# Kernel optimization log

Measured on AMD Instinct MI355X. Metric: run time of the kernel, lower is better.

Reference implementation:

```python
import jax, jax.numpy as jnp
import numpy as np

V, D, Q = 50000, 300, 200  # vocab, word_embedding_dim, query_vector_dim
ALPHA = 0.2  # LeakyReLU negative slope


def _gat(h, W, a):
    # h: [N, D]; full adjacency of ones -> mask is a no-op, softmax over all pairs
    d = a.shape[0] // 2
    Wh = h @ W                                        # [N, D]
    e = jax.nn.leaky_relu(Wh @ a[:d] + (Wh @ a[d:]).T, ALPHA)  # [N, N]
    att = jax.nn.softmax(e, axis=1)                   # [N, N]
    return jax.nn.elu(att @ Wh)                       # [N, D]


def _additive_attention(x, lin_w, lin_b, query):
    # x: [B, S, D] -> [B, D]
    temp = jnp.tanh(x @ lin_w.T + lin_b)              # [B, S, Q]
    w = jax.nn.softmax(temp @ query, axis=1)          # [B, S, 1]
    return jnp.sum(x * w, axis=1)


def _news_encode(titles, emb, W, a, lin_w, lin_b, query):
    # titles: [B, L] int; dropout p=0 (eval)
    v = emb[titles]                                   # [B, L, D]
    b, l, d = v.shape
    g = _gat(v.reshape(b * l, d), W, a).reshape(b, l, d)
    return _additive_attention(g, lin_w, lin_b, query)  # [B, D]


def setup_inputs() -> dict:
    key = jax.random.key(0)
    ks = jax.random.split(key, 13)
    B, C, H, L = 64, 5, 50, 32
    f = jnp.float32
    return {
        "candidate_titles": jax.random.randint(ks[0], (B, C, L), 0, V, dtype=jnp.int32),
        "clicked_titles": jax.random.randint(ks[1], (B, H, L), 0, V, dtype=jnp.int32),
        "emb": jax.random.normal(ks[2], (V, D), f) * 0.1,
        "news_W": jax.random.normal(ks[3], (D, D), f) * (1.0 / np.sqrt(D)),
        "news_a": jax.random.normal(ks[4], (2 * D, 1), f) * (1.0 / np.sqrt(2 * D)),
        "news_lin_w": jax.random.normal(ks[5], (Q, D), f) * (1.0 / np.sqrt(D)),
        "news_lin_b": jnp.zeros((Q,), f),
        "news_query": jax.random.normal(ks[6], (Q, 1), f) * (1.0 / np.sqrt(Q)),
        "user_W": jax.random.normal(ks[7], (D, D), f) * (1.0 / np.sqrt(D)),
        "user_a": jax.random.normal(ks[8], (2 * D, 1), f) * (1.0 / np.sqrt(2 * D)),
        "user_lin_w": jax.random.normal(ks[9], (Q, D), f) * (1.0 / np.sqrt(D)),
        "user_lin_b": jnp.zeros((Q,), f),
        "user_query": jax.random.normal(ks[10], (Q, 1), f) * (1.0 / np.sqrt(Q)),
    }


def reference(candidate_titles, clicked_titles, emb, news_W, news_a,
              news_lin_w, news_lin_b, news_query, user_W, user_a,
              user_lin_w, user_lin_b, user_query):
    enc = lambda t: _news_encode(t, emb, news_W, news_a, news_lin_w, news_lin_b, news_query)
    # per-news-item encoding (each item gets its own full-batch GAT)
    cand = jax.vmap(enc)(candidate_titles.transpose(1, 0, 2)).transpose(1, 0, 2)   # [B, C, D]
    clicked = jax.vmap(enc)(clicked_titles.transpose(1, 0, 2)).transpose(1, 0, 2)  # [B, H, D]
    # user encoder: GAT over flattened [B*H, D] with full adjacency
    b, h, d = clicked.shape
    g = _gat(clicked.reshape(b * h, d), user_W, user_a).reshape(b, h, d)
    user = _additive_attention(g, user_lin_w, user_lin_b, user_query)              # [B, D]
    # dot-product click predictor
    return jnp.einsum('bcd,bd->bc', cand, user)                                    # [B, C]
```

## Files before the change

kernel.cpp:

```cpp
#include <hip/hip_runtime.h>
#include <hip/hip_bf16.h>

#define BN_B 64
#define NC 5
#define NH 50
#define NL 32
#define DD 300
#define QQ 200
#define NVOC 50000
#define NGAT 55
#define NROW 2048
#define NUSR 3200
#define NUSR_PAD 3328
#define CW 304
#define NT_NEWS 128
#define NT_USER 208
#define NB_NEWS 128
#define NB_USER 200
#define GSTR 320
#define NTILES_N 13
#define KTILES 10
#define BPELT (NTILES_N * KTILES * 64)
#define WNT 19
#define WKT 10
#define WPELT (WNT * WKT * 64)
#define KTBYTES (NTILES_N * 64 * 16)
#define KTCHUNK (KTBYTES / 16)

typedef short bf16x8 __attribute__((ext_vector_type(8)));
typedef short bf16x4 __attribute__((ext_vector_type(4)));
typedef float f32x4 __attribute__((ext_vector_type(4)));

static __device__ __forceinline__ float bf2f(short s) {
  return __uint_as_float(((unsigned)(unsigned short)s) << 16);
}

__global__ __launch_bounds__(256) void k_packW(const float* __restrict__ W0,
                                               const float* __restrict__ W1,
                                               __hip_bfloat16* __restrict__ h0,
                                               __hip_bfloat16* __restrict__ l0,
                                               __hip_bfloat16* __restrict__ h1,
                                               __hip_bfloat16* __restrict__ l1) {
  const float* Wm = blockIdx.y ? W1 : W0;
  __hip_bfloat16* Bhi = blockIdx.y ? h1 : h0;
  __hip_bfloat16* Blo = blockIdx.y ? l1 : l0;
  int e = blockIdx.x * 256 + threadIdx.x;
  if (e >= WPELT) return;
  int lane = e & 63, nt = (e >> 6) % WNT, kt = (e >> 6) / WNT;
  int n = nt * 16 + (lane & 15);
  int k0 = kt * 32 + (lane >> 4) * 8;
  __hip_bfloat16 hv[8], lv[8];
#pragma unroll
  for (int j = 0; j < 8; ++j) {
    int k = k0 + j;
    float v = (k < DD && n < DD) ? Wm[(size_t)k * DD + n] : 0.f;
    __hip_bfloat16 h = __float2bfloat16(v);
    hv[j] = h;
    lv[j] = __float2bfloat16(v - __bfloat162float(h));
  }
  *(bf16x8*)(Bhi + (size_t)e * 8) = *(const bf16x8*)hv;
  *(bf16x8*)(Blo + (size_t)e * 8) = *(const bf16x8*)lv;
}

__global__ __launch_bounds__(256) void k_packB(const float* __restrict__ lw0,
                                               const float* __restrict__ lw1,
                                               __hip_bfloat16* __restrict__ B0,
                                               __hip_bfloat16* __restrict__ B1) {
  const float* lw = blockIdx.y ? lw1 : lw0;
  __hip_bfloat16* Bp = blockIdx.y ? B1 : B0;
  int e = blockIdx.x * 256 + threadIdx.x;
  if (e >= BPELT) return;
  int lane = e & 63, nt = (e >> 6) % NTILES_N, kt = (e >> 6) / NTILES_N;
  int n = nt * 16 + (lane & 15);
  int k0 = kt * 32 + (lane >> 4) * 8;
  __hip_bfloat16 vals[8];
#pragma unroll
  for (int j = 0; j < 8; ++j) {
    int k = k0 + j;
    float v = (n < QQ && k < DD) ? lw[(size_t)n * DD + k] : 0.f;
    vals[j] = __float2bfloat16(v);
  }
  *(bf16x8*)(Bp + (size_t)e * 8) = *(const bf16x8*)vals;
}

__global__ __launch_bounds__(256) void k_gemm_mfma(const float* __restrict__ A,
                                                   const __hip_bfloat16* __restrict__ Bhi,
                                                   const __hip_bfloat16* __restrict__ Blo,
                                                   const float* __restrict__ avec,
                                                   float* __restrict__ C,
                                                   float* __restrict__ s1o,
                                                   float* __restrict__ s2o, int M) {
  const int tid = threadIdx.x;
  const int wave = tid >> 6, lane = tid & 63;
  const int quad = lane >> 4, l16 = lane & 15;
  const int rowA = blockIdx.x * 64 + wave * 16 + l16;
  const float* ar = A + (size_t)rowA * DD;
  f32x4 acc[WNT];
#pragma unroll
  for (int nt = 0; nt < WNT; ++nt) acc[nt] = (f32x4){0.f, 0.f, 0.f, 0.f};

  for (int kt = 0; kt < WKT; ++kt) {
    const int k0 = kt * 32 + quad * 8;
    float av[8];
    if (rowA < M && k0 + 8 <= DD) {
      float4 v0 = *(const float4*)(ar + k0);
      float4 v1 = *(const float4*)(ar + k0 + 4);
      av[0] = v0.x; av[1] = v0.y; av[2] = v0.z; av[3] = v0.w;
      av[4] = v1.x; av[5] = v1.y; av[6] = v1.z; av[7] = v1.w;
    } else {
#pragma unroll
      for (int j = 0; j < 8; ++j) {
        int k = k0 + j;
        av[j] = (rowA < M && k < DD) ? ar[k] : 0.f;
      }
    }
    __hip_bfloat16 hv[8], lv[8];
#pragma unroll
    for (int j = 0; j < 8; ++j) {
      __hip_bfloat16 h = __float2bfloat16(av[j]);
      hv[j] = h;
      lv[j] = __float2bfloat16(av[j] - __bfloat162float(h));
    }
    const bf16x8 ah = *(const bf16x8*)hv;
    const bf16x8 al = *(const bf16x8*)lv;
    const bf16x8* bh = (const bf16x8*)Bhi + (size_t)(kt * WNT) * 64 + lane;
    const bf16x8* bl = (const bf16x8*)Blo + (size_t)(kt * WNT) * 64 + lane;
#pragma unroll
    for (int nt = 0; nt < WNT; ++nt) {
      bf16x8 bhf = bh[nt * 64], blf = bl[nt * 64];
      acc[nt] = __builtin_amdgcn_mfma_f32_16x16x32_bf16(ah, bhf, acc[nt], 0, 0, 0);
      acc[nt] = __builtin_amdgcn_mfma_f32_16x16x32_bf16(al, bhf, acc[nt], 0, 0, 0);
      acc[nt] = __builtin_amdgcn_mfma_f32_16x16x32_bf16(ah, blf, acc[nt], 0, 0, 0);
    }
  }
  const int mbase = blockIdx.x * 64 + wave * 16 + quad * 4;
#pragma unroll
  for (int nt = 0; nt < WNT; ++nt) {
    int n = nt * 16 + l16;
    if (n < DD) {
#pragma unroll
      for (int r = 0; r < 4; ++r) {
        int mr = mbase + r;
        if (mr < M) C[(size_t)mr * DD + n] = acc[nt][r];
      }
    }
  }
  float a1v[WNT], a2v[WNT];
#pragma unroll
  for (int nt = 0; nt < WNT; ++nt) {
    int n = nt * 16 + l16;
    a1v[nt] = (n < DD) ? avec[n] : 0.f;
    a2v[nt] = (n < DD) ? avec[DD + n] : 0.f;
  }
#pragma unroll
  for (int r = 0; r < 4; ++r) {
    float p1 = 0.f, p2 = 0.f;
#pragma unroll
    for (int nt = 0; nt < WNT; ++nt) {
      p1 = fmaf(acc[nt][r], a1v[nt], p1);
      p2 = fmaf(acc[nt][r], a2v[nt], p2);
    }
    p1 += __shfl_xor(p1, 1, 64); p1 += __shfl_xor(p1, 2, 64);
    p1 += __shfl_xor(p1, 4, 64); p1 += __shfl_xor(p1, 8, 64);
    p2 += __shfl_xor(p2, 1, 64); p2 += __shfl_xor(p2, 2, 64);
    p2 += __shfl_xor(p2, 4, 64); p2 += __shfl_xor(p2, 8, 64);
    int mr = mbase + r;
    if (l16 == 0 && mr < M) { s1o[mr] = p1; s2o[mr] = p2; }
  }
}

__global__ __launch_bounds__(1024) void k_sort2(const int* __restrict__ cand,
                                                const int* __restrict__ clicked,
                                                const float* __restrict__ s2src,
                                                const float* __restrict__ s1src,
                                                int* __restrict__ perm,
                                                float* __restrict__ E1, float* __restrict__ E02,
                                                int* __restrict__ rlist, float* __restrict__ rs1,
                                                int* __restrict__ boff,
                                                int mode, int N, int SZ, int Epad, int NB) {
  __shared__ float sval[4096];
  __shared__ int spay[4096];
  __shared__ int cnt[224];
  __shared__ int ofs[224];
  const int m = blockIdx.x;
  const int tid = threadIdx.x;
  int* perm_g = perm + (size_t)m * Epad;
  float* E1_g = E1 + (size_t)m * Epad;
  float* E02_g = E02 + (size_t)m * Epad;

  for (int i = tid; i < SZ; i += 1024) {
    float v; int p;
    if (mode == 0) {
      int b = i >> 5, l = i & 31;
      int tok = (m < NC) ? cand[b * (NC * NL) + m * NL + l]
                         : clicked[b * (NH * NL) + (m - NC) * NL + l];
      v = s2src[tok]; p = tok;
    } else {
      if (i < N) { v = s2src[i]; p = i; } else { v = __builtin_inff(); p = 0; }
    }
    sval[i] = v; spay[i] = p;
  }
  __syncthreads();
  for (int k = 2; k <= SZ; k <<= 1) {
    for (int j = k >> 1; j > 0; j >>= 1) {
      for (int i = tid; i < SZ; i += 1024) {
        int ixj = i ^ j;
        if (ixj > i) {
          bool asc = ((i & k) == 0);
          float a = sval[i], bb = sval[ixj];
          bool sw = asc ? (a > bb) : (a < bb);
          if (sw) {
            sval[i] = bb; sval[ixj] = a;
            int t = spay[i]; spay[i] = spay[ixj]; spay[ixj] = t;
          }
        }
      }
      __syncthreads();
    }
  }
  for (int i = tid; i < Epad; i += 1024) {
    E1_g[i] = (i < N) ? expf(sval[i]) : 0.f;
    E02_g[i] = (i < N) ? expf(0.2f * sval[i]) : 0.f;
    perm_g[i] = spay[i];
  }
  __syncthreads();
  for (int t = tid; t <= NB; t += 1024) cnt[t] = 0;
  __syncthreads();
  int* kil = spay;
  for (int r = tid; r < N; r += 1024) {
    int tok;
    if (mode == 0) {
      int b = r >> 5, l = r & 31;
      tok = (m < NC) ? cand[b * (NC * NL) + m * NL + l]
                     : clicked[b * (NH * NL) + (m - NC) * NL + l];
    } else tok = r;
    float tau = -s1src[tok];
    int lo = 0, hi = N;
    while (lo < hi) { int mid = (lo + hi) >> 1; if (sval[mid] <= tau) lo = mid + 1; else hi = mid; }
    kil[r] = lo;
    atomicAdd(&cnt[lo >> 4], 1);
  }
  __syncthreads();
  if (tid == 0) {
    int run = 0;
    for (int t = 0; t <= NB; ++t) { ofs[t] = run; run += cnt[t]; cnt[t] = ofs[t]; }
  }
  __syncthreads();
  int* rlist_g = rlist + (size_t)m * N;
  float* rs1_g = rs1 + (size_t)m * N;
  for (int r = tid; r < N; r += 1024) {
    int ki = kil[r];
    int pos = atomicAdd(&cnt[ki >> 4], 1);
    rlist_g[pos] = (ki << 16) | r;
    int tok;
    if (mode == 0) {
      int b = r >> 5, l = r & 31;
      tok = (m < NC) ? cand[b * (NC * NL) + m * NL + l]
                     : clicked[b * (NH * NL) + (m - NC) * NL + l];
    } else tok = r;
    rs1_g[pos] = s1src[tok];
  }
  int* boff_g = boff + (size_t)m * (NB + 2);
  for (int t = tid; t <= NB; t += 1024) boff_g[t] = ofs[t];
  if (tid == 0) boff_g[NB + 1] = N;
}

__global__ __launch_bounds__(320) void k_scan(const float* __restrict__ base,
                                              const int* __restrict__ perm,
                                              const float* __restrict__ E1,
                                              const float* __restrict__ E02,
                                              float* __restrict__ C1, float* __restrict__ C02,
                                              float* __restrict__ T1, float* __restrict__ T02,
                                              int Epad, int cstride, int nkc) {
  const int g = blockIdx.y, kc = blockIdx.x;
  const int col = threadIdx.x;
  const int* perm_g = perm + (size_t)g * Epad;
  const float* E1_g = E1 + (size_t)g * Epad;
  const float* E02_g = E02 + (size_t)g * Epad;
  float* C1_g = C1 + (size_t)g * cstride * CW;
  float* C02_g = C02 + (size_t)g * cstride * CW;
  const bool datacol = (col < DD);
  const float wden = (col == DD) ? 1.f : 0.f;
  float acc1 = 0.f, acc2 = 0.f;
  const int k0 = kc * 256;
#pragma unroll 8
  for (int kk = 0; kk < 256; ++kk) {
    int k = k0 + kk;
    int tok = perm_g[k];
    float e1 = E1_g[k], e02 = E02_g[k];
    float w = datacol ? base[(size_t)tok * DD + col] : wden;
    acc1 = fmaf(e1, w, acc1);
    acc2 = fmaf(e02, w, acc2);
    if ((kk & 15) == 15) {
      int t = (k + 1) >> 4;
      if (col < CW) { C1_g[(size_t)t * CW + col] = acc1; C02_g[(size_t)t * CW + col] = acc2; }
    }
  }
  if (col < CW) {
    T1[((size_t)g * nkc + kc) * CW + col] = acc1;
    T02[((size_t)g * nkc + kc) * CW + col] = acc2;
  }
}

__global__ __launch_bounds__(320) void k_rows2(
    const float* __restrict__ base,
    const int* __restrict__ perm, const float* __restrict__ E1, const float* __restrict__ E02,
    const float* __restrict__ C1, const float* __restrict__ C02,
    const float* __restrict__ T1, const float* __restrict__ T02,
    const int* __restrict__ rlist, const float* __restrict__ rs1,
    const int* __restrict__ boff,
    __hip_bfloat16* __restrict__ gout,
    int N, int NT, int Epad, int NB, int nkc) {
  __shared__ float U1[16][CW];
  __shared__ float U02[16][CW];
  __shared__ int tokL[16];
  __shared__ float e1L[16], e02L[16];
  const int t = blockIdx.x, g = blockIdx.y;
  const int col = threadIdx.x;
  const int* boff_g = boff + (size_t)g * (NB + 2);
  const int i0 = boff_g[t], i1 = boff_g[t + 1];
  if (i0 >= i1) return;
  const int* perm_g = perm + (size_t)g * Epad;
  const float* E1_g = E1 + (size_t)g * Epad;
  const float* E02_g = E02 + (size_t)g * Epad;
  if (col < 16) {
    int idx = t * 16 + col;
    bool v = idx < N;
    tokL[col] = v ? perm_g[idx] : 0;
    e1L[col] = v ? E1_g[idx] : 0.f;
    e02L[col] = v ? E02_g[idx] : 0.f;
  }
  __syncthreads();
  if (col < CW) {
    const int kc = (t == 0) ? 0 : ((t - 1) >> 4);
    float tot1 = 0.f, pre1 = 0.f, pre02 = 0.f;
#pragma unroll
    for (int c = 0; c < 13; ++c) {
      if (c < nkc) {
        float tv = T1[((size_t)g * nkc + c) * CW + col];
        tot1 += tv;
        if (c < kc) {
          pre1 += tv;
          pre02 += T02[((size_t)g * nkc + c) * CW + col];
        }
      }
    }
    if (t > 0) {
      pre1 += C1[((size_t)g * (NT + 1) + t) * CW + col];
      pre02 += C02[((size_t)g * (NT + 1) + t) * CW + col];
    }
    float u1 = tot1 - pre1;
    float u02 = pre02;
    float wv[16];
#pragma unroll
    for (int j = 0; j < 16; ++j) {
      if (col < DD) wv[j] = ((t * 16 + j) < N) ? base[(size_t)tokL[j] * DD + col] : 0.f;
      else wv[j] = (col == DD) ? 1.f : 0.f;
    }
#pragma unroll
    for (int j = 0; j < 16; ++j) {
      U1[j][col] = u1; U02[j][col] = u02;
      u1 = fmaf(-e1L[j], wv[j], u1);
      u02 = fmaf(e02L[j], wv[j], u02);
    }
  }
  __syncthreads();
  const int wave = col >> 6, lane = col & 63;
  const int* rlist_g = rlist + (size_t)g * N;
  const float* rs1_g = rs1 + (size_t)g * N;
  for (int i = i0 + wave; i < i1; i += 5) {
    int e = rlist_g[i];
    int r = e & 0xffff, nr = (e >> 16) & 15;
    float s1 = rs1_g[i];
    float es1 = expf(s1), es02 = expf(0.2f * s1);
    float den = es1 * U1[nr][DD] + es02 * U02[nr][DD];
    float rden = 1.f / den;
    __hip_bfloat16* gr = gout + ((size_t)g * N + r) * GSTR;
#pragma unroll
    for (int cc = 0; cc < 2; ++cc) {
      int ch = lane + 64 * cc;
      if (ch < 80) {
        short ov[4];
        if (ch < 75) {
          const int c0 = ch * 4;
          float4 u1v = *(const float4*)&U1[nr][c0];
          float4 u2v = *(const float4*)&U02[nr][c0];
          float n0 = fmaf(es1, u1v.x, es02 * u2v.x) * rden;
          float n1 = fmaf(es1, u1v.y, es02 * u2v.y) * rden;
          float n2 = fmaf(es1, u1v.z, es02 * u2v.z) * rden;
          float n3 = fmaf(es1, u1v.w, es02 * u2v.w) * rden;
          float g0 = (n0 > 0.f) ? n0 : expm1f(n0);
          float g1 = (n1 > 0.f) ? n1 : expm1f(n1);
          float g2 = (n2 > 0.f) ? n2 : expm1f(n2);
          float g3 = (n3 > 0.f) ? n3 : expm1f(n3);
          __hip_bfloat16 h0 = __float2bfloat16(g0), h1 = __float2bfloat16(g1);
          __hip_bfloat16 h2 = __float2bfloat16(g2), h3 = __float2bfloat16(g3);
          ov[0] = *(short*)&h0; ov[1] = *(short*)&h1;
          ov[2] = *(short*)&h2; ov[3] = *(short*)&h3;
        } else {
          ov[0] = ov[1] = ov[2] = ov[3] = 0;
        }
        *(bf16x4*)(gr + ch * 4) = *(bf16x4*)ov;
      }
    }
  }
}

__global__ __launch_bounds__(512) void k_logits_attn(
    const __hip_bfloat16* __restrict__ g, const __hip_bfloat16* __restrict__ Bp,
    const float* __restrict__ lin_b, const float* __restrict__ query,
    float* __restrict__ cand_enc, float* __restrict__ clicked_enc) {
  __shared__ __align__(16) short Bs[2][NTILES_N * 512];
  __shared__ float lg[128];
  __shared__ float wgt[128];
  __shared__ float accw[8][GSTR];
  const int tid = threadIdx.x;
  const int wave = tid >> 6, lane = tid & 63;
  const int quad = lane >> 4, l16 = lane & 15;
  const int m = blockIdx.x >> 4;
  const int rbase = (blockIdx.x & 15) * 128;
  const __hip_bfloat16* grow =
      g + ((size_t)m * NROW + rbase + wave * 16 + l16) * GSTR + quad * 8;
  bf16x8 afr[KTILES];
#pragma unroll
  for (int kt = 0; kt < KTILES; ++kt) afr[kt] = *(const bf16x8*)(grow + kt * 32);

  const float4* bsrc = (const float4*)Bp;
  float4* bdst0 = (float4*)&Bs[0][0];
  float4* bdst1 = (float4*)&Bs[1][0];
  float4 st0, st1;
  {
    st0 = bsrc[tid];
    if (tid < KTCHUNK - 512) st1 = bsrc[512 + tid];
    bdst0[tid] = st0;
    if (tid < KTCHUNK - 512) bdst0[512 + tid] = st1;
    st0 = bsrc[KTCHUNK + tid];
    if (tid < KTCHUNK - 512) st1 = bsrc[KTCHUNK + 512 + tid];
  }
  __syncthreads();
  f32x4 acc[NTILES_N];
#pragma unroll
  for (int nt = 0; nt < NTILES_N; ++nt) acc[nt] = (f32x4){0.f, 0.f, 0.f, 0.f};
  int c = 0;
  for (int kt = 0; kt < KTILES; ++kt) {
    const bf16x8* bp = (const bf16x8*)&Bs[c][0] + lane;
#pragma unroll
    for (int nt = 0; nt < NTILES_N; ++nt)
      acc[nt] = __builtin_amdgcn_mfma_f32_16x16x32_bf16(afr[kt], bp[nt * 64], acc[nt], 0, 0, 0);
    if (kt < KTILES - 1) {
      __syncthreads();
      float4* bd = c ? bdst0 : bdst1;
      bd[tid] = st0;
      if (tid < KTCHUNK - 512) bd[512 + tid] = st1;
      if (kt < KTILES - 2) {
        st0 = bsrc[(size_t)(kt + 2) * KTCHUNK + tid];
        if (tid < KTCHUNK - 512) st1 = bsrc[(size_t)(kt + 2) * KTCHUNK + 512 + tid];
      }
      __syncthreads();
      c ^= 1;
    }
  }
  float part[4] = {0.f, 0.f, 0.f, 0.f};
#pragma unroll
  for (int nt = 0; nt < NTILES_N; ++nt) {
    const int n = nt * 16 + l16;
    const float qv = (n < QQ) ? query[n] : 0.f;
    const float bv = (n < QQ) ? lin_b[n] : 0.f;
#pragma unroll
    for (int r = 0; r < 4; ++r)
      part[r] = fmaf(tanhf(acc[nt][r] + bv), qv, part[r]);
  }
#pragma unroll
  for (int r = 0; r < 4; ++r) {
    float p = part[r];
    p += __shfl_xor(p, 1, 64); p += __shfl_xor(p, 2, 64);
    p += __shfl_xor(p, 4, 64); p += __shfl_xor(p, 8, 64);
    if (l16 == 0) lg[wave * 16 + quad * 4 + r] = p;
  }
  __syncthreads();
  if (tid < 128) {
    float v = lg[tid];
    float mx = v;
    mx = fmaxf(mx, __shfl_xor(mx, 1, 64)); mx = fmaxf(mx, __shfl_xor(mx, 2, 64));
    mx = fmaxf(mx, __shfl_xor(mx, 4, 64)); mx = fmaxf(mx, __shfl_xor(mx, 8, 64));
    mx = fmaxf(mx, __shfl_xor(mx, 16, 64));
    float e = expf(v - mx), sm = e;
    sm += __shfl_xor(sm, 1, 64); sm += __shfl_xor(sm, 2, 64);
    sm += __shfl_xor(sm, 4, 64); sm += __shfl_xor(sm, 8, 64);
    sm += __shfl_xor(sm, 16, 64);
    wgt[tid] = e / sm;
  }
  __syncthreads();
  const float w = wgt[wave * 16 + l16];
#pragma unroll
  for (int kt = 0; kt < KTILES; ++kt) {
#pragma unroll
    for (int j = 0; j < 8; ++j) {
      float v = bf2f(afr[kt][j]) * w;
      v += __shfl_xor(v, 1, 64); v += __shfl_xor(v, 2, 64);
      v += __shfl_xor(v, 4, 64); v += __shfl_xor(v, 8, 64);
      if (l16 == 0) accw[wave][kt * 32 + quad * 8 + j] = v;
    }
  }
  __syncthreads();
  const int b0 = rbase >> 5;
  for (int idx = tid; idx < 4 * DD; idx += 512) {
    int j = idx / DD, cc = idx % DD;
    float* op = (m < NC) ? (cand_enc + ((size_t)(b0 + j) * NC + m) * DD)
                         : (clicked_enc + ((size_t)(b0 + j) * NH + (m - NC)) * DD);
    op[cc] = accw[2 * j][cc] + accw[2 * j + 1][cc];
  }
}

__global__ __launch_bounds__(256) void k_user_attn(
    const __hip_bfloat16* __restrict__ g, const __hip_bfloat16* __restrict__ Bp,
    const float* __restrict__ lin_b, const float* __restrict__ query,
    const float* __restrict__ cand_enc, float* __restrict__ out) {
  __shared__ float lg[64];
  __shared__ float wgt[64];
  __shared__ float accw[4][GSTR];
  __shared__ float uenc[CW];
  __shared__ float wred[4];
  const int b = blockIdx.x, tid = threadIdx.x;
  const int wave = tid >> 6, lane = tid & 63;
  const int quad = lane >> 4, l16 = lane & 15;
  const int rl = wave * 16 + l16;
  const int rclamp = (rl < NH) ? rl : 0;
  const __hip_bfloat16* grow = g + ((size_t)b * NH + rclamp) * GSTR + quad * 8;
  bf16x8 afr[KTILES];
#pragma unroll
  for (int kt = 0; kt < KTILES; ++kt) afr[kt] = *(const bf16x8*)(grow + kt * 32);
  f32x4 acc[NTILES_N];
#pragma unroll
  for (int nt = 0; nt < NTILES_N; ++nt) acc[nt] = (f32x4){0.f, 0.f, 0.f, 0.f};
  for (int kt = 0; kt < KTILES; ++kt) {
    const bf16x8* bp = (const bf16x8*)Bp + (size_t)kt * NTILES_N * 64 + lane;
#pragma unroll
    for (int nt = 0; nt < NTILES_N; ++nt)
      acc[nt] = __builtin_amdgcn_mfma_f32_16x16x32_bf16(afr[kt], bp[nt * 64], acc[nt], 0, 0, 0);
  }
  float part[4] = {0.f, 0.f, 0.f, 0.f};
#pragma unroll
  for (int nt = 0; nt < NTILES_N; ++nt) {
    const int n = nt * 16 + l16;
    const float qv = (n < QQ) ? query[n] : 0.f;
    const float bv = (n < QQ) ? lin_b[n] : 0.f;
#pragma unroll
    for (int r = 0; r < 4; ++r)
      part[r] = fmaf(tanhf(acc[nt][r] + bv), qv, part[r]);
  }
#pragma unroll
  for (int r = 0; r < 4; ++r) {
    float p = part[r];
    p += __shfl_xor(p, 1, 64); p += __shfl_xor(p, 2, 64);
    p += __shfl_xor(p, 4, 64); p += __shfl_xor(p, 8, 64);
    if (l16 == 0) lg[wave * 16 + quad * 4 + r] = p;
  }
  __syncthreads();
  if (tid < 64) {
    float v = (tid < NH) ? lg[tid] : -3.4e38f;
    float mx = v;
    for (int o = 32; o; o >>= 1) mx = fmaxf(mx, __shfl_xor(mx, o, 64));
    float e = (tid < NH) ? expf(v - mx) : 0.f;
    float sm = e;
    for (int o = 32; o; o >>= 1) sm += __shfl_xor(sm, o, 64);
    wgt[tid] = (tid < NH) ? e / sm : 0.f;
  }
  __syncthreads();
  const float w = (rl < NH) ? wgt[rl] : 0.f;
#pragma unroll
  for (int kt = 0; kt < KTILES; ++kt) {
#pragma unroll
    for (int j = 0; j < 8; ++j) {
      float v = bf2f(afr[kt][j]) * w;
      v += __shfl_xor(v, 1, 64); v += __shfl_xor(v, 2, 64);
      v += __shfl_xor(v, 4, 64); v += __shfl_xor(v, 8, 64);
      if (l16 == 0) accw[wave][kt * 32 + quad * 8 + j] = v;
    }
  }
  __syncthreads();
  for (int c = tid; c < DD; c += 256)
    uenc[c] = accw[0][c] + accw[1][c] + accw[2][c] + accw[3][c];
  __syncthreads();
  for (int c5 = 0; c5 < NC; ++c5) {
    const float* cp = cand_enc + ((size_t)b * NC + c5) * DD;
    float s = 0.f;
    for (int d = tid; d < DD; d += 256) s = fmaf(uenc[d], cp[d], s);
    for (int o = 32; o; o >>= 1) s += __shfl_xor(s, o, 64);
    if (lane == 0) wred[wave] = s;
    __syncthreads();
    if (tid == 0) out[b * NC + c5] = wred[0] + wred[1] + wred[2] + wred[3];
    __syncthreads();
  }
}

extern "C" void kernel_launch(void* const* d_in, const int* in_sizes, int n_in,
                              void* d_out, int out_size, void* d_ws, size_t ws_size,
                              hipStream_t stream) {
  const int* cand = (const int*)d_in[0];
  const int* clicked = (const int*)d_in[1];
  const float* emb = (const float*)d_in[2];
  const float* news_W = (const float*)d_in[3];
  const float* news_a = (const float*)d_in[4];
  const float* news_lw = (const float*)d_in[5];
  const float* news_lb = (const float*)d_in[6];
  const float* news_q = (const float*)d_in[7];
  const float* user_W = (const float*)d_in[8];
  const float* user_a = (const float*)d_in[9];
  const float* user_lw = (const float*)d_in[10];
  const float* user_lb = (const float*)d_in[11];
  const float* user_q = (const float*)d_in[12];
  float* out = (float*)d_out;

  float* W = (float*)d_ws;
  size_t o = 0;
  auto nxt = [&](size_t n) { size_t c = o; o += (n + 63) & ~(size_t)63; return c; };
  float* EW = W + nxt((size_t)NVOC * DD);
  float* s1v = W + nxt(NVOC);
  float* s2v = W + nxt(NVOC);
  int* perm = (int*)(W + nxt((size_t)NGAT * NROW));
  float* E1 = W + nxt((size_t)NGAT * NROW);
  float* E02 = W + nxt((size_t)NGAT * NROW);
  float* C1 = W + nxt((size_t)NGAT * (NT_NEWS + 1) * CW);
  float* C02 = W + nxt((size_t)NGAT * (NT_NEWS + 1) * CW);
  float* T1N = W + nxt((size_t)NGAT * 8 * CW);
  float* T02N = W + nxt((size_t)NGAT * 8 * CW);
  int* rlistN = (int*)(W + nxt((size_t)NGAT * NROW));
  float* rs1N = W + nxt((size_t)NGAT * NROW);
  int* boffN = (int*)(W + nxt((size_t)NGAT * (NB_NEWS + 2)));
  float* cand_enc = W + nxt((size_t)BN_B * NC * DD);
  float* clicked_enc = W + nxt((size_t)BN_B * NH * DD);
  float* WhU = W + nxt((size_t)NUSR * DD);
  float* s1u = W + nxt(NUSR);
  float* s2u = W + nxt(NUSR);
  int* permU = (int*)(W + nxt(NUSR_PAD));
  float* E1U = W + nxt(NUSR_PAD);
  float* E02U = W + nxt(NUSR_PAD);
  float* C1U = W + nxt((size_t)(NT_USER + 1) * CW);
  float* C02U = W + nxt((size_t)(NT_USER + 1) * CW);
  float* T1U = W + nxt((size_t)13 * CW);
  float* T02U = W + nxt((size_t)13 * CW);
  int* rlistU = (int*)(W + nxt(NUSR));
  float* rs1U = W + nxt(NUSR);
  int* boffU = (int*)(W + nxt(NB_USER + 2));
  __hip_bfloat16* BpN = (__hip_bfloat16*)(W + nxt((size_t)BPELT * 8 / 2));
  __hip_bfloat16* BpU = (__hip_bfloat16*)(W + nxt((size_t)BPELT * 8 / 2));
  __hip_bfloat16* WhiN = (__hip_bfloat16*)(W + nxt((size_t)WPELT * 8 / 2));
  __hip_bfloat16* WloN = (__hip_bfloat16*)(W + nxt((size_t)WPELT * 8 / 2));
  __hip_bfloat16* WhiU = (__hip_bfloat16*)(W + nxt((size_t)WPELT * 8 / 2));
  __hip_bfloat16* WloU = (__hip_bfloat16*)(W + nxt((size_t)WPELT * 8 / 2));
  __hip_bfloat16* g_news = (__hip_bfloat16*)(W + nxt((size_t)NGAT * NROW * GSTR / 2));
  __hip_bfloat16* g_user = (__hip_bfloat16*)(W + nxt((size_t)NUSR * GSTR / 2));

  const int packgrid = (BPELT + 255) / 256;
  const int packWgrid = (WPELT + 255) / 256;

  k_packW<<<dim3(packWgrid, 2), 256, 0, stream>>>(news_W, user_W, WhiN, WloN, WhiU, WloU);
  k_packB<<<dim3(packgrid, 2), 256, 0, stream>>>(news_lw, user_lw, BpN, BpU);
  k_gemm_mfma<<<(NVOC + 63) / 64, 256, 0, stream>>>(emb, WhiN, WloN, news_a, EW, s1v, s2v, NVOC);
  k_sort2<<<NGAT, 1024, 0, stream>>>(cand, clicked, s2v, s1v, perm, E1, E02,
                                     rlistN, rs1N, boffN, 0, NROW, NROW, NROW, NB_NEWS);
  k_scan<<<dim3(8, NGAT), 320, 0, stream>>>(EW, perm, E1, E02, C1, C02, T1N, T02N,
                                            NROW, NT_NEWS + 1, 8);
  k_rows2<<<dim3(NB_NEWS + 1, NGAT), 320, 0, stream>>>(EW, perm, E1, E02, C1, C02, T1N, T02N,
                                                       rlistN, rs1N, boffN, g_news,
                                                       NROW, NT_NEWS, NROW, NB_NEWS, 8);
  k_logits_attn<<<NGAT * NROW / 128, 512, 0, stream>>>(g_news, BpN, news_lb, news_q,
                                                       cand_enc, clicked_enc);
  k_gemm_mfma<<<(NUSR + 63) / 64, 256, 0, stream>>>(clicked_enc, WhiU, WloU, user_a,
                                                    WhU, s1u, s2u, NUSR);
  k_sort2<<<1, 1024, 0, stream>>>(nullptr, nullptr, s2u, s1u, permU, E1U, E02U,
                                  rlistU, rs1U, boffU, 1, NUSR, 4096, NUSR_PAD, NB_USER);
  k_scan<<<dim3(13, 1), 320, 0, stream>>>(WhU, permU, E1U, E02U, C1U, C02U, T1U, T02U,
                                          NUSR_PAD, NT_USER + 1, 13);
  k_rows2<<<dim3(NB_USER + 1, 1), 320, 0, stream>>>(WhU, permU, E1U, E02U, C1U, C02U, T1U, T02U,
                                                    rlistU, rs1U, boffU, g_user,
                                                    NUSR, NT_USER, NUSR_PAD, NB_USER, 13);
  k_user_attn<<<BN_B, 256, 0, stream>>>(g_user, BpU, user_lb, user_q, cand_enc, out);
}
```

Baseline: 745.4 us.

## Replace user-GAT sort/scan path with dense bf16 attention GEMM; LDS-stage W tiles

```diff
diff --git a/kernel.cpp b/kernel.cpp
--- a/kernel.cpp
+++ b/kernel.cpp
@@ -11,12 +11,9 @@
 #define NGAT 55
 #define NROW 2048
 #define NUSR 3200
-#define NUSR_PAD 3328
 #define CW 304
 #define NT_NEWS 128
-#define NT_USER 208
 #define NB_NEWS 128
-#define NB_USER 200
 #define GSTR 320
 #define NTILES_N 13
 #define KTILES 10
@@ -26,6 +23,13 @@
 #define WPELT (WNT * WKT * 64)
 #define KTBYTES (NTILES_N * 64 * 16)
 #define KTCHUNK (KTBYTES / 16)
+#define GCH 1216
+#define GKCH 2432
+#define PKT 104
+#define PNT 19
+#define PPELT (PKT * PNT * 64)
+#define PSTR 3328
+#define PJT 416
 
 typedef short bf16x8 __attribute__((ext_vector_type(8)));
 typedef short bf16x4 __attribute__((ext_vector_type(4)));
@@ -83,22 +87,47 @@
   *(bf16x8*)(Bp + (size_t)e * 8) = *(const bf16x8*)vals;
 }
 
-__global__ __launch_bounds__(256) void k_gemm_mfma(const float* __restrict__ A,
+__global__ __launch_bounds__(512) void k_gemm_mfma(const float* __restrict__ A,
                                                    const __hip_bfloat16* __restrict__ Bhi,
                                                    const __hip_bfloat16* __restrict__ Blo,
                                                    const float* __restrict__ avec,
                                                    float* __restrict__ C,
                                                    float* __restrict__ s1o,
                                                    float* __restrict__ s2o, int M) {
+  __shared__ __align__(16) float4 Bs4[2][GKCH];
   const int tid = threadIdx.x;
   const int wave = tid >> 6, lane = tid & 63;
   const int quad = lane >> 4, l16 = lane & 15;
-  const int rowA = blockIdx.x * 64 + wave * 16 + l16;
+  const int rowA = blockIdx.x * 128 + wave * 16 + l16;
   const float* ar = A + (size_t)rowA * DD;
+  const float4* hsrc = (const float4*)Bhi;
+  const float4* lsrc = (const float4*)Blo;
+  float4 st[5];
+
+#define LOADKT(kt)                                                         \
+  {                                                                        \
+    _Pragma("unroll") for (int s = 0; s < 5; ++s) {                        \
+      int idx = s * 512 + tid;                                             \
+      if (idx < GKCH)                                                      \
+        st[s] = (idx < GCH) ? hsrc[(size_t)(kt)*GCH + idx]                 \
+                            : lsrc[(size_t)(kt)*GCH + idx - GCH];          \
+    }                                                                      \
+  }
+#define STOREBUF(b)                                                        \
+  {                                                                        \
+    _Pragma("unroll") for (int s = 0; s < 5; ++s) {                        \
+      int idx = s * 512 + tid;                                             \
+      if (idx < GKCH) Bs4[b][idx] = st[s];                                 \
+    }                                                                      \
+  }
+
+  LOADKT(0); STOREBUF(0); LOADKT(1);
+  __syncthreads();
+
   f32x4 acc[WNT];
 #pragma unroll
   for (int nt = 0; nt < WNT; ++nt) acc[nt] = (f32x4){0.f, 0.f, 0.f, 0.f};
-
+  int c = 0;
   for (int kt = 0; kt < WKT; ++kt) {
     const int k0 = kt * 32 + quad * 8;
     float av[8];
@@ -123,8 +152,8 @@
     }
     const bf16x8 ah = *(const bf16x8*)hv;
     const bf16x8 al = *(const bf16x8*)lv;
-    const bf16x8* bh = (const bf16x8*)Bhi + (size_t)(kt * WNT) * 64 + lane;
-    const bf16x8* bl = (const bf16x8*)Blo + (size_t)(kt * WNT) * 64 + lane;
+    const bf16x8* bh = (const bf16x8*)&Bs4[c][0] + lane;
+    const bf16x8* bl = (const bf16x8*)&Bs4[c][GCH] + lane;
 #pragma unroll
     for (int nt = 0; nt < WNT; ++nt) {
       bf16x8 bhf = bh[nt * 64], blf = bl[nt * 64];
@@ -132,8 +161,15 @@
       acc[nt] = __builtin_amdgcn_mfma_f32_16x16x32_bf16(al, bhf, acc[nt], 0, 0, 0);
       acc[nt] = __builtin_amdgcn_mfma_f32_16x16x32_bf16(ah, blf, acc[nt], 0, 0, 0);
     }
-  }
-  const int mbase = blockIdx.x * 64 + wave * 16 + quad * 4;
+    if (kt < WKT - 1) {
+      __syncthreads();
+      STOREBUF(c ^ 1);
+      if (kt < WKT - 2) LOADKT(kt + 2);
+      __syncthreads();
+      c ^= 1;
+    }
+  }
+  const int mbase = blockIdx.x * 128 + wave * 16 + quad * 4;
 #pragma unroll
   for (int nt = 0; nt < WNT; ++nt) {
     int n = nt * 16 + l16;
@@ -167,6 +203,8 @@
     int mr = mbase + r;
     if (l16 == 0 && mr < M) { s1o[mr] = p1; s2o[mr] = p2; }
   }
+#undef LOADKT
+#undef STOREBUF
 }
 
 __global__ __launch_bounds__(1024) void k_sort2(const int* __restrict__ cand,
@@ -177,33 +215,27 @@
                                                 float* __restrict__ E1, float* __restrict__ E02,
                                                 int* __restrict__ rlist, float* __restrict__ rs1,
                                                 int* __restrict__ boff,
-                                                int mode, int N, int SZ, int Epad, int NB) {
-  __shared__ float sval[4096];
-  __shared__ int spay[4096];
+                                                int N, int NB) {
+  __shared__ float sval[2048];
+  __shared__ int spay[2048];
   __shared__ int cnt[224];
   __shared__ int ofs[224];
   const int m = blockIdx.x;
   const int tid = threadIdx.x;
-  int* perm_g = perm + (size_t)m * Epad;
-  float* E1_g = E1 + (size_t)m * Epad;
-  float* E02_g = E02 + (size_t)m * Epad;
-
-  for (int i = tid; i < SZ; i += 1024) {
-    float v; int p;
-    if (mode == 0) {
-      int b = i >> 5, l = i & 31;
-      int tok = (m < NC) ? cand[b * (NC * NL) + m * NL + l]
-                         : clicked[b * (NH * NL) + (m - NC) * NL + l];
-      v = s2src[tok]; p = tok;
-    } else {
-      if (i < N) { v = s2src[i]; p = i; } else { v = __builtin_inff(); p = 0; }
-    }
-    sval[i] = v; spay[i] = p;
-  }
-  __syncthreads();
-  for (int k = 2; k <= SZ; k <<= 1) {
+  int* perm_g = perm + (size_t)m * N;
+  float* E1_g = E1 + (size_t)m * N;
+  float* E02_g = E02 + (size_t)m * N;
+
+  for (int i = tid; i < N; i += 1024) {
+    int b = i >> 5, l = i & 31;
+    int tok = (m < NC) ? cand[b * (NC * NL) + m * NL + l]
+                       : clicked[b * (NH * NL) + (m - NC) * NL + l];
+    sval[i] = s2src[tok]; spay[i] = tok;
+  }
+  __syncthreads();
+  for (int k = 2; k <= N; k <<= 1) {
     for (int j = k >> 1; j > 0; j >>= 1) {
-      for (int i = tid; i < SZ; i += 1024) {
+      for (int i = tid; i < N; i += 1024) {
         int ixj = i ^ j;
         if (ixj > i) {
           bool asc = ((i & k) == 0);
@@ -218,9 +250,9 @@
       __syncthreads();
     }
   }
-  for (int i = tid; i < Epad; i += 1024) {
-    E1_g[i] = (i < N) ? expf(sval[i]) : 0.f;
-    E02_g[i] = (i < N) ? expf(0.2f * sval[i]) : 0.f;
+  for (int i = tid; i < N; i += 1024) {
+    E1_g[i] = expf(sval[i]);
+    E02_g[i] = expf(0.2f * sval[i]);
     perm_g[i] = spay[i];
   }
   __syncthreads();
@@ -228,12 +260,9 @@
   __syncthreads();
   int* kil = spay;
   for (int r = tid; r < N; r += 1024) {
-    int tok;
-    if (mode == 0) {
-      int b = r >> 5, l = r & 31;
-      tok = (m < NC) ? cand[b * (NC * NL) + m * NL + l]
-                     : clicked[b * (NH * NL) + (m - NC) * NL + l];
-    } else tok = r;
+    int b = r >> 5, l = r & 31;
+    int tok = (m < NC) ? cand[b * (NC * NL) + m * NL + l]
+                       : clicked[b * (NH * NL) + (m - NC) * NL + l];
     float tau = -s1src[tok];
     int lo = 0, hi = N;
     while (lo < hi) { int mid = (lo + hi) >> 1; if (sval[mid] <= tau) lo = mid + 1; else hi = mid; }
@@ -252,12 +281,9 @@
     int ki = kil[r];
     int pos = atomicAdd(&cnt[ki >> 4], 1);
     rlist_g[pos] = (ki << 16) | r;
-    int tok;
-    if (mode == 0) {
-      int b = r >> 5, l = r & 31;
-      tok = (m < NC) ? cand[b * (NC * NL) + m * NL + l]
-                     : clicked[b * (NH * NL) + (m - NC) * NL + l];
-    } else tok = r;
+    int b = r >> 5, l = r & 31;
+    int tok = (m < NC) ? cand[b * (NC * NL) + m * NL + l]
+                       : clicked[b * (NH * NL) + (m - NC) * NL + l];
     rs1_g[pos] = s1src[tok];
   }
   int* boff_g = boff + (size_t)m * (NB + 2);
@@ -372,7 +398,7 @@
     int e = rlist_g[i];
     int r = e & 0xffff, nr = (e >> 16) & 15;
     float s1 = rs1_g[i];
-    float es1 = expf(s1), es02 = expf(0.2f * s1);
+    float es1 = __expf(s1), es02 = __expf(0.2f * s1);
     float den = es1 * U1[nr][DD] + es02 * U02[nr][DD];
     float rden = 1.f / den;
     __hip_bfloat16* gr = gout + ((size_t)g * N + r) * GSTR;
@@ -389,10 +415,10 @@
           float n1 = fmaf(es1, u1v.y, es02 * u2v.y) * rden;
           float n2 = fmaf(es1, u1v.z, es02 * u2v.z) * rden;
           float n3 = fmaf(es1, u1v.w, es02 * u2v.w) * rden;
-          float g0 = (n0 > 0.f) ? n0 : expm1f(n0);
-          float g1 = (n1 > 0.f) ? n1 : expm1f(n1);
-          float g2 = (n2 > 0.f) ? n2 : expm1f(n2);
-          float g3 = (n3 > 0.f) ? n3 : expm1f(n3);
+          float g0 = (n0 > 0.f) ? n0 : (__expf(n0) - 1.f);
+          float g1 = (n1 > 0.f) ? n1 : (__expf(n1) - 1.f);
+          float g2 = (n2 > 0.f) ? n2 : (__expf(n2) - 1.f);
+          float g3 = (n3 > 0.f) ? n3 : (__expf(n3) - 1.f);
           __hip_bfloat16 h0 = __float2bfloat16(g0), h1 = __float2bfloat16(g1);
           __hip_bfloat16 h2 = __float2bfloat16(g2), h3 = __float2bfloat16(g3);
           ov[0] = *(short*)&h0; ov[1] = *(short*)&h1;
@@ -510,6 +536,120 @@
                          : (clicked_enc + ((size_t)(b0 + j) * NH + (m - NC)) * DD);
     op[cc] = accw[2 * j][cc] + accw[2 * j + 1][cc];
   }
+}
+
+__global__ __launch_bounds__(256) void k_pbuild(const float* __restrict__ s1u,
+                                                const float* __restrict__ s2u,
+                                                __hip_bfloat16* __restrict__ P) {
+  int gid = blockIdx.x * 256 + threadIdx.x;
+  if (gid >= NUSR * PJT) return;
+  int i = gid / PJT, jg = gid % PJT;
+  int j0 = jg * 8;
+  float s1 = s1u[i];
+  __hip_bfloat16 ov[8];
+#pragma unroll
+  for (int q = 0; q < 8; ++q) {
+    int j = j0 + q;
+    float w = 0.f;
+    if (j < NUSR) {
+      float s = s1 + s2u[j];
+      w = __expf(s > 0.f ? s : 0.2f * s);
+    }
+    ov[q] = __float2bfloat16(w);
+  }
+  *(bf16x8*)(P + (size_t)i * PSTR + j0) = *(const bf16x8*)ov;
+}
+
+__global__ __launch_bounds__(256) void k_packP(const float* __restrict__ Wh,
+                                               __hip_bfloat16* __restrict__ Bp) {
+  int e = blockIdx.x * 256 + threadIdx.x;
+  if (e >= PPELT) return;
+  int lane = e & 63, nt = (e >> 6) % PNT, kt = (e >> 6) / PNT;
+  int n = nt * 16 + (lane & 15);
+  int k0 = kt * 32 + (lane >> 4) * 8;
+  __hip_bfloat16 vals[8];
+#pragma unroll
+  for (int j = 0; j < 8; ++j) {
+    int k = k0 + j;
+    float v = 0.f;
+    if (k < NUSR) {
+      if (n < DD) v = Wh[(size_t)k * DD + n];
+      else if (n == DD) v = 1.f;
+    }
+    vals[j] = __float2bfloat16(v);
+  }
+  *(bf16x8*)(Bp + (size_t)e * 8) = *(const bf16x8*)vals;
+}
+
+__global__ __launch_bounds__(256) void k_pgemm(const __hip_bfloat16* __restrict__ P,
+                                               const __hip_bfloat16* __restrict__ Bp,
+                                               __hip_bfloat16* __restrict__ gout) {
+  __shared__ __align__(16) float4 Bs4[2][PNT * 64];
+  const int tid = threadIdx.x;
+  const int wave = tid >> 6, lane = tid & 63;
+  const int quad = lane >> 4, l16 = lane & 15;
+  const int rowA = blockIdx.x * 64 + wave * 16 + l16;
+  const __hip_bfloat16* ar = P + (size_t)rowA * PSTR;
+  const float4* bsrc = (const float4*)Bp;
+  const int NCH = PNT * 64;
+  float4 st[5];
+
+#define PLOADKT(kt)                                                        \
+  {                                                                        \
+    _Pragma("unroll") for (int s = 0; s < 5; ++s) {                        \
+      int idx = s * 256 + tid;                                             \
+      if (idx < NCH) st[s] = bsrc[(size_t)(kt)*NCH + idx];                 \
+    }                                                                      \
+  }
+#define PSTOREBUF(b)                                                       \
+  {                                                                        \
+    _Pragma("unroll") for (int s = 0; s < 5; ++s) {                        \
+      int idx = s * 256 + tid;                                             \
+      if (idx < NCH) Bs4[b][idx] = st[s];                                  \
+    }                                                                      \
+  }
+
+  PLOADKT(0); PSTOREBUF(0); PLOADKT(1);
+  __syncthreads();
+  f32x4 acc[PNT];
+#pragma unroll
+  for (int nt = 0; nt < PNT; ++nt) acc[nt] = (f32x4){0.f, 0.f, 0.f, 0.f};
+  int c = 0;
+  for (int kt = 0; kt < PKT; ++kt) {
+    bf16x8 a = *(const bf16x8*)(ar + kt * 32 + quad * 8);
+    const bf16x8* bp = (const bf16x8*)&Bs4[c][0] + lane;
+#pragma unroll
+    for (int nt = 0; nt < PNT; ++nt)
+      acc[nt] = __builtin_amdgcn_mfma_f32_16x16x32_bf16(a, bp[nt * 64], acc[nt], 0, 0, 0);
+    if (kt < PKT - 1) {
+      __syncthreads();
+      PSTOREBUF(c ^ 1);
+      if (kt < PKT - 2) PLOADKT(kt + 2);
+      __syncthreads();
+      c ^= 1;
+    }
+  }
+  const int rbase = blockIdx.x * 64 + wave * 16 + quad * 4;
+#pragma unroll
+  for (int r = 0; r < 4; ++r) {
+    float den = __shfl(acc[18][r], (lane & 48) | 12, 64);
+    float rden = 1.f / den;
+    __hip_bfloat16* gr = gout + (size_t)(rbase + r) * GSTR;
+#pragma unroll
+    for (int nt = 0; nt < PNT; ++nt) {
+      int n = nt * 16 + l16;
+      if (n < DD) {
+        float v = acc[nt][r] * rden;
+        float gg = (v > 0.f) ? v : (__expf(v) - 1.f);
+        gr[n] = __float2bfloat16(gg);
+      } else {
+        gr[n] = __float2bfloat16(0.f);
+      }
+    }
+    gr[304 + l16] = __float2bfloat16(0.f);
+  }
+#undef PLOADKT
+#undef PSTOREBUF
 }
 
 __global__ __launch_bounds__(256) void k_user_attn(
@@ -633,22 +773,14 @@
   float* WhU = W + nxt((size_t)NUSR * DD);
   float* s1u = W + nxt(NUSR);
   float* s2u = W + nxt(NUSR);
-  int* permU = (int*)(W + nxt(NUSR_PAD));
-  float* E1U = W + nxt(NUSR_PAD);
-  float* E02U = W + nxt(NUSR_PAD);
-  float* C1U = W + nxt((size_t)(NT_USER + 1) * CW);
-  float* C02U = W + nxt((size_t)(NT_USER + 1) * CW);
-  float* T1U = W + nxt((size_t)13 * CW);
-  float* T02U = W + nxt((size_t)13 * CW);
-  int* rlistU = (int*)(W + nxt(NUSR));
-  float* rs1U = W + nxt(NUSR);
-  int* boffU = (int*)(W + nxt(NB_USER + 2));
   __hip_bfloat16* BpN = (__hip_bfloat16*)(W + nxt((size_t)BPELT * 8 / 2));
   __hip_bfloat16* BpU = (__hip_bfloat16*)(W + nxt((size_t)BPELT * 8 / 2));
   __hip_bfloat16* WhiN = (__hip_bfloat16*)(W + nxt((size_t)WPELT * 8 / 2));
   __hip_bfloat16* WloN = (__hip_bfloat16*)(W + nxt((size_t)WPELT * 8 / 2));
   __hip_bfloat16* WhiU = (__hip_bfloat16*)(W + nxt((size_t)WPELT * 8 / 2));
   __hip_bfloat16* WloU = (__hip_bfloat16*)(W + nxt((size_t)WPELT * 8 / 2));
+  __hip_bfloat16* Pm = (__hip_bfloat16*)(W + nxt((size_t)NUSR * PSTR / 2));
+  __hip_bfloat16* BpP = (__hip_bfloat16*)(W + nxt((size_t)PPELT * 8 / 2));
   __hip_bfloat16* g_news = (__hip_bfloat16*)(W + nxt((size_t)NGAT * NROW * GSTR / 2));
   __hip_bfloat16* g_user = (__hip_bfloat16*)(W + nxt((size_t)NUSR * GSTR / 2));
 
@@ -657,9 +789,10 @@
 
   k_packW<<<dim3(packWgrid, 2), 256, 0, stream>>>(news_W, user_W, WhiN, WloN, WhiU, WloU);
   k_packB<<<dim3(packgrid, 2), 256, 0, stream>>>(news_lw, user_lw, BpN, BpU);
-  k_gemm_mfma<<<(NVOC + 63) / 64, 256, 0, stream>>>(emb, WhiN, WloN, news_a, EW, s1v, s2v, NVOC);
+  k_gemm_mfma<<<(NVOC + 127) / 128, 512, 0, stream>>>(emb, WhiN, WloN, news_a,
+                                                      EW, s1v, s2v, NVOC);
   k_sort2<<<NGAT, 1024, 0, stream>>>(cand, clicked, s2v, s1v, perm, E1, E02,
-                                     rlistN, rs1N, boffN, 0, NROW, NROW, NROW, NB_NEWS);
+                                     rlistN, rs1N, boffN, NROW, NB_NEWS);
   k_scan<<<dim3(8, NGAT), 320, 0, stream>>>(EW, perm, E1, E02, C1, C02, T1N, T02N,
                                             NROW, NT_NEWS + 1, 8);
   k_rows2<<<dim3(NB_NEWS + 1, NGAT), 320, 0, stream>>>(EW, perm, E1, E02, C1, C02, T1N, T02N,
@@ -667,14 +800,10 @@
                                                        NROW, NT_NEWS, NROW, NB_NEWS, 8);
   k_logits_attn<<<NGAT * NROW / 128, 512, 0, stream>>>(g_news, BpN, news_lb, news_q,
                                                        cand_enc, clicked_enc);
-  k_gemm_mfma<<<(NUSR + 63) / 64, 256, 0, stream>>>(clicked_enc, WhiU, WloU, user_a,
-                                                    WhU, s1u, s2u, NUSR);
-  k_sort2<<<1, 1024, 0, stream>>>(nullptr, nullptr, s2u, s1u, permU, E1U, E02U,
-                                  rlistU, rs1U, boffU, 1, NUSR, 4096, NUSR_PAD, NB_USER);
-  k_scan<<<dim3(13, 1), 320, 0, stream>>>(WhU, permU, E1U, E02U, C1U, C02U, T1U, T02U,
-                                          NUSR_PAD, NT_USER + 1, 13);
-  k_rows2<<<dim3(NB_USER + 1, 1), 320, 0, stream>>>(WhU, permU, E1U, E02U, C1U, C02U, T1U, T02U,
-                                                    rlistU, rs1U, boffU, g_user,
-                                                    NUSR, NT_USER, NUSR_PAD, NB_USER, 13);
+  k_gemm_mfma<<<(NUSR + 127) / 128, 512, 0, stream>>>(clicked_enc, WhiU, WloU, user_a,
+                                                      WhU, s1u, s2u, NUSR);
+  k_packP<<<(PPELT + 255) / 256, 256, 0, stream>>>(WhU, BpP);
+  k_pbuild<<<(NUSR * PJT + 255) / 256, 256, 0, stream>>>(s1u, s2u, Pm);
+  k_pgemm<<<NUSR / 64, 256, 0, stream>>>(Pm, BpP, g_user);
   k_user_attn<<<BN_B, 256, 0, stream>>>(g_user, BpU, user_lb, user_q, cand_enc, out);
 }
```

Result: slower. 867.5 us (+16.4%).
